# Optimization experiments

Measured on AMD Instinct MI355X. Metric: run time of the kernel, lower is better.

The kernel has to match this reference:

```python
import jax, jax.numpy as jnp
import numpy as np

V, D, CTX, NL = 32000, 1024, 2048, 2
B, T = 4, 2048
EPS = 1e-5


def _layer_norm(x, gamma, beta):
    mu = jnp.mean(x, axis=-1, keepdims=True)
    var = jnp.var(x, axis=-1, keepdims=True)  # biased, matches unbiased=False
    return gamma * (x - mu) / jnp.sqrt(var + EPS) + beta


def setup_inputs() -> dict:
    key = jax.random.key(0)
    ks = jax.random.split(key, 12)
    s = 0.02
    return {
        "x": jax.random.randint(ks[0], (B, T), 0, V),
        "emb": jax.random.normal(ks[1], (V, D), jnp.float32) * s,
        "pos": jax.random.normal(ks[2], (CTX, D), jnp.float32) * s,
        "wq": jax.random.normal(ks[3], (NL, D, D), jnp.float32) * s,
        "wk": jax.random.normal(ks[4], (NL, D, D), jnp.float32) * s,
        "wv": jax.random.normal(ks[5], (NL, D, D), jnp.float32) * s,
        "wo": jax.random.normal(ks[6], (NL, D, D), jnp.float32) * s,
        "wup": jax.random.normal(ks[7], (NL, D, 4 * D), jnp.float32) * s,
        "bup": jnp.zeros((NL, 4 * D), jnp.float32),
        "wdown": jax.random.normal(ks[8], (NL, 4 * D, D), jnp.float32) * s,
        "bdown": jnp.zeros((NL, D), jnp.float32),
        "ga": jnp.ones((NL, D), jnp.float32),
        "ba": jnp.zeros((NL, D), jnp.float32),
        "gm": jnp.ones((NL, D), jnp.float32),
        "bm": jnp.zeros((NL, D), jnp.float32),
    }


def reference(x, emb, pos, wq, wk, wv, wo, wup, bup, wdown, bdown, ga, ba, gm, bm):
    Bx, Tx = x.shape
    d_model = emb.shape[-1]
    inv_sqrt_d = 1.0 / jnp.sqrt(jnp.asarray(d_model, jnp.float32))
    h = emb[x] + pos[:Tx][None, :, :]           # [B,T,D]
    causal = jnp.tril(jnp.ones((Tx, Tx), bool))  # [T,T]
    neg_inf = jnp.asarray(-jnp.inf, h.dtype)
    n_layers = wq.shape[0]
    for l in range(n_layers):
        residual = h
        q = h @ wq[l]
        k = h @ wk[l]
        v = h @ wv[l]
        wei = jnp.einsum('btd,bsd->bts', q, k) * inv_sqrt_d  # [B,T,T]
        wei = jnp.where(causal[None], wei, neg_inf)
        attn = jax.nn.softmax(wei, axis=-1)
        out = jnp.einsum('bts,bsd->btd', attn, v)
        z = out @ wo[l]
        h = _layer_norm(residual + z, ga[l], ba[l])
        m = jax.nn.relu(h @ wup[l] + bup[l]) @ wdown[l] + bdown[l]
        h = _layer_norm(h + m, gm[l], bm[l])
    return h
```

## Files before the change

### kernel.cpp

```cpp
#include <hip/hip_runtime.h>
#include <stdint.h>

typedef unsigned short u16;
typedef short short8 __attribute__((ext_vector_type(8)));
typedef short short4v __attribute__((ext_vector_type(4)));
typedef float f32x4 __attribute__((ext_vector_type(4)));

#define DEV static __device__ __forceinline__

DEV u16 f2bf(float x) {
    union { float f; uint32_t u; } v; v.f = x;
    uint32_t r = v.u + 0x7FFFu + ((v.u >> 16) & 1u);
    return (u16)(r >> 16);
}
DEV float bf2f(u16 h) {
    union { uint32_t u; float f; } v; v.u = ((uint32_t)h) << 16;
    return v.f;
}

DEV void gload_lds16(const u16* g, u16* l) {
    __builtin_amdgcn_global_load_lds(
        (__attribute__((address_space(1))) void*)g,
        (__attribute__((address_space(3))) void*)l, 16, 0, 0);
}

enum { F_RELU = 1, F_ACCUM = 2, F_CSKIP = 4, F_CKLIM = 8 };

__global__ __launch_bounds__(256, 2)
void gemm_bt(const u16* __restrict__ A, const u16* __restrict__ B,
             float* __restrict__ Cf, u16* __restrict__ Cb,
             const float* __restrict__ bias,
             int M, int N, int K, int lda, int ldb, int ldc,
             long long sA, long long sB, long long sC,
             float scale, int flags)
{
    const int tm = blockIdx.x, tn = blockIdx.y, bz = blockIdx.z;
    if ((flags & F_CSKIP) && tn > tm) return;
    A += (long long)bz * sA;
    B += (long long)bz * sB;
    const long long coff = (long long)bz * sC;

    __shared__ u16 As[128 * 32];
    __shared__ u16 Bs[128 * 32];

    const int tid = threadIdx.x;
    const int lane = tid & 63, w = tid >> 6;
    const int wr = w >> 1, wc = w & 1;
    const int l15 = lane & 15, l4 = lane >> 4;

    f32x4 acc[4][4];
    const f32x4 z4 = {0.f, 0.f, 0.f, 0.f};
#pragma unroll
    for (int m = 0; m < 4; ++m)
#pragma unroll
        for (int n = 0; n < 4; ++n) acc[m][n] = z4;

    int kend = K;
    if (flags & F_CKLIM) { int ke = (tm + 1) * 128; if (ke < kend) kend = ke; }

    const u16* Abase = A + (long long)tm * 128 * lda;
    const u16* Bbase = B + (long long)tn * 128 * ldb;

    for (int k0 = 0; k0 < kend; k0 += 32) {
#pragma unroll
        for (int i = 0; i < 2; ++i) {
            const int e0 = (i * 4 + w) * 512;
            const int e  = e0 + lane * 8;
            const int row = e >> 5, col = e & 31;
            gload_lds16(Abase + (long long)row * lda + (k0 + col), (u16*)As + e0);
            gload_lds16(Bbase + (long long)row * ldb + (k0 + col), (u16*)Bs + e0);
        }
        __syncthreads();

        short8 af[4], bfr[4];
#pragma unroll
        for (int m = 0; m < 4; ++m)
            af[m] = *(const short8*)&As[(wr * 64 + m * 16 + l15) * 32 + l4 * 8];
#pragma unroll
        for (int n = 0; n < 4; ++n)
            bfr[n] = *(const short8*)&Bs[(wc * 64 + n * 16 + l15) * 32 + l4 * 8];
#pragma unroll
        for (int m = 0; m < 4; ++m)
#pragma unroll
            for (int n = 0; n < 4; ++n)
                acc[m][n] = __builtin_amdgcn_mfma_f32_16x16x32_bf16(af[m], bfr[n], acc[m][n], 0, 0, 0);
        __syncthreads();
    }

#pragma unroll
    for (int n = 0; n < 4; ++n) {
        const int c = tn * 128 + wc * 64 + n * 16 + l15;
        const float bv = bias ? bias[c] : 0.0f;
#pragma unroll
        for (int m = 0; m < 4; ++m) {
            const int r0 = tm * 128 + wr * 64 + m * 16 + l4 * 4;
#pragma unroll
            for (int j = 0; j < 4; ++j) {
                float v = acc[m][n][j] * scale + bv;
                if (flags & F_RELU) v = fmaxf(v, 0.0f);
                const long long off = coff + (long long)(r0 + j) * ldc + c;
                if (flags & F_ACCUM) v += Cf[off];
                if (Cf) Cf[off] = v;
                if (Cb) Cb[off] = f2bf(v);
            }
        }
    }
}

__global__ void transpose_f2b(const float* __restrict__ in, u16* __restrict__ out, int R, int C)
{
    __shared__ float tile[32][33];
    const int tx = threadIdx.x, ty = threadIdx.y;
    const int gx = blockIdx.x, gy = blockIdx.y;
#pragma unroll
    for (int i = 0; i < 4; ++i)
        tile[ty + i * 8][tx] = in[(long long)(gy * 32 + ty + i * 8) * C + gx * 32 + tx];
    __syncthreads();
#pragma unroll
    for (int i = 0; i < 4; ++i)
        out[(long long)(gx * 32 + ty + i * 8) * R + gy * 32 + tx] = f2bf(tile[tx][ty + i * 8]);
}

__global__ void transpose_b2b(const u16* __restrict__ in, u16* __restrict__ out,
                              int R, int C, long long sIn, long long sOut)
{
    __shared__ u16 tile[32][34];
    in  += (long long)blockIdx.z * sIn;
    out += (long long)blockIdx.z * sOut;
    const int tx = threadIdx.x, ty = threadIdx.y;
    const int gx = blockIdx.x, gy = blockIdx.y;
#pragma unroll
    for (int i = 0; i < 4; ++i)
        tile[ty + i * 8][tx] = in[(long long)(gy * 32 + ty + i * 8) * C + gx * 32 + tx];
    __syncthreads();
#pragma unroll
    for (int i = 0; i < 4; ++i)
        out[(long long)(gx * 32 + ty + i * 8) * R + gy * 32 + tx] = tile[tx][ty + i * 8];
}

__global__ __launch_bounds__(256)
void embed_kernel(const int* __restrict__ x, const float* __restrict__ emb,
                  const float* __restrict__ pos, float* __restrict__ h32, u16* __restrict__ hbf)
{
    const long long row = blockIdx.x;
    const int t = (int)(row & 2047);
    const int idx = x[row];
    const int tid = threadIdx.x;
    const float4 e = ((const float4*)(emb + (long long)idx * 1024))[tid];
    const float4 p = ((const float4*)(pos + (long long)t * 1024))[tid];
    float y0 = e.x + p.x, y1 = e.y + p.y, y2 = e.z + p.z, y3 = e.w + p.w;
    float4 o; o.x = y0; o.y = y1; o.z = y2; o.w = y3;
    ((float4*)(h32 + row * 1024))[tid] = o;
    short4v ob = { (short)f2bf(y0), (short)f2bf(y1), (short)f2bf(y2), (short)f2bf(y3) };
    *(short4v*)(hbf + row * 1024 + tid * 4) = ob;
}

__global__ __launch_bounds__(256)
void ln_kernel(const float* __restrict__ a, const float* __restrict__ b,
               const float* __restrict__ gamma, const float* __restrict__ beta,
               float* __restrict__ o32, u16* __restrict__ obf)
{
    const long long row = blockIdx.x;
    const int tid = threadIdx.x, lane = tid & 63, w = tid >> 6;
    const float4 xa = ((const float4*)(a + row * 1024))[tid];
    const float4 xb = ((const float4*)(b + row * 1024))[tid];
    float x0 = xa.x + xb.x, x1 = xa.y + xb.y, x2 = xa.z + xb.z, x3 = xa.w + xb.w;
    float s = x0 + x1 + x2 + x3;
    float q = x0 * x0 + x1 * x1 + x2 * x2 + x3 * x3;
#pragma unroll
    for (int o = 32; o; o >>= 1) { s += __shfl_xor(s, o, 64); q += __shfl_xor(q, o, 64); }
    __shared__ float red[8];
    if (lane == 0) { red[w] = s; red[4 + w] = q; }
    __syncthreads();
    s = red[0] + red[1] + red[2] + red[3];
    q = red[4] + red[5] + red[6] + red[7];
    const float mu = s * (1.0f / 1024.0f);
    const float var = q * (1.0f / 1024.0f) - mu * mu;
    const float rs = rsqrtf(var + 1e-5f);
    const float4 g  = ((const float4*)gamma)[tid];
    const float4 be = ((const float4*)beta)[tid];
    float y0 = (x0 - mu) * rs * g.x + be.x;
    float y1 = (x1 - mu) * rs * g.y + be.y;
    float y2 = (x2 - mu) * rs * g.z + be.z;
    float y3 = (x3 - mu) * rs * g.w + be.w;
    float4 o; o.x = y0; o.y = y1; o.z = y2; o.w = y3;
    ((float4*)(o32 + row * 1024))[tid] = o;
    short4v ob = { (short)f2bf(y0), (short)f2bf(y1), (short)f2bf(y2), (short)f2bf(y3) };
    *(short4v*)(obf + row * 1024 + tid * 4) = ob;
}

__global__ __launch_bounds__(256)
void softmax_causal(u16* __restrict__ SP)
{
    const long long row = blockIdx.x;
    const int t = (int)(row & 2047);
    u16* p = SP + row * 2048;
    const int tid = threadIdx.x, lane = tid & 63, w = tid >> 6;

    short8 v = *(const short8*)&p[tid * 8];
    float x[8];
#pragma unroll
    for (int j = 0; j < 8; ++j) {
        const int c = tid * 8 + j;
        x[j] = (c <= t) ? bf2f((u16)v[j]) : -1e30f;
    }
    float mx = x[0];
#pragma unroll
    for (int j = 1; j < 8; ++j) mx = fmaxf(mx, x[j]);
#pragma unroll
    for (int o = 32; o; o >>= 1) mx = fmaxf(mx, __shfl_xor(mx, o, 64));
    __shared__ float red[8];
    if (lane == 0) red[w] = mx;
    __syncthreads();
    mx = fmaxf(fmaxf(red[0], red[1]), fmaxf(red[2], red[3]));

    float s = 0.f;
#pragma unroll
    for (int j = 0; j < 8; ++j) {
        const float e = (tid * 8 + j <= t) ? exp2f((x[j] - mx) * 1.44269504f) : 0.f;
        x[j] = e; s += e;
    }
#pragma unroll
    for (int o = 32; o; o >>= 1) s += __shfl_xor(s, o, 64);
    if (lane == 0) red[4 + w] = s;
    __syncthreads();
    s = red[4] + red[5] + red[6] + red[7];
    const float inv = 1.0f / s;

    short8 ov;
#pragma unroll
    for (int j = 0; j < 8; ++j) ov[j] = (short)f2bf(x[j] * inv);
    *(short8*)&p[tid * 8] = ov;
}

extern "C" void kernel_launch(void* const* d_in, const int* in_sizes, int n_in,
                              void* d_out, int out_size, void* d_ws, size_t ws_size,
                              hipStream_t stream)
{
    (void)in_sizes; (void)n_in; (void)out_size; (void)ws_size;
    const int Dd = 1024, T_ = 2048, B_ = 4, NLl = 2, M = B_ * T_;
    const float inv_sqrt_d = 0.03125f;

    const int*   x     = (const int*)  d_in[0];
    const float* emb   = (const float*)d_in[1];
    const float* pos   = (const float*)d_in[2];
    const float* wq    = (const float*)d_in[3];
    const float* wk    = (const float*)d_in[4];
    const float* wv    = (const float*)d_in[5];
    const float* wo    = (const float*)d_in[6];
    const float* wup   = (const float*)d_in[7];
    const float* bup   = (const float*)d_in[8];
    const float* wdown = (const float*)d_in[9];
    const float* bdown = (const float*)d_in[10];
    const float* ga    = (const float*)d_in[11];
    const float* ba    = (const float*)d_in[12];
    const float* gm    = (const float*)d_in[13];
    const float* bm    = (const float*)d_in[14];

    char* ws = (char*)d_ws;
    size_t off = 0;
    auto alloc = [&](size_t bytes) -> void* {
        void* p = ws + off; off += (bytes + 255) & ~(size_t)255; return p;
    };
    float* h32  = (float*)alloc((size_t)M * Dd * 4);
    u16*   hbf  = (u16*)  alloc((size_t)M * Dd * 2);
    float* z32  = (float*)alloc((size_t)M * Dd * 4);
    u16*   qbf  = (u16*)  alloc((size_t)M * Dd * 2);
    u16*   kbf  = (u16*)  alloc((size_t)M * Dd * 2);
    u16*   vbf  = (u16*)  alloc((size_t)M * Dd * 2);
    u16*   vtbf = (u16*)  alloc((size_t)M * Dd * 2);
    u16*   SP   = (u16*)  alloc((size_t)B_ * T_ * T_ * 2);
    u16*   ubf  = (u16*)  alloc((size_t)M * 2048 * 2);
    u16*   wtb  = (u16*)  alloc((size_t)12 * 1024 * 1024 * 2);

    u16* wq_t    = wtb;
    u16* wk_t    = wtb + 1 * 1048576;
    u16* wv_t    = wtb + 2 * 1048576;
    u16* wo_t    = wtb + 3 * 1048576;
    u16* wup_t   = wtb + 4 * 1048576;
    u16* wdown_t = wtb + 8 * 1048576;

    dim3 blk(256);
    dim3 tblk(32, 8);

    embed_kernel<<<M, blk, 0, stream>>>(x, emb, pos, h32, hbf);

    for (int l = 0; l < NLl; ++l) {
        const float* wq_l    = wq    + (size_t)l * Dd * Dd;
        const float* wk_l    = wk    + (size_t)l * Dd * Dd;
        const float* wv_l    = wv    + (size_t)l * Dd * Dd;
        const float* wo_l    = wo    + (size_t)l * Dd * Dd;
        const float* wup_l   = wup   + (size_t)l * Dd * 4096;
        const float* wdown_l = wdown + (size_t)l * 4096 * Dd;

        transpose_f2b<<<dim3(32, 32),  tblk, 0, stream>>>(wq_l, wq_t, 1024, 1024);
        transpose_f2b<<<dim3(32, 32),  tblk, 0, stream>>>(wk_l, wk_t, 1024, 1024);
        transpose_f2b<<<dim3(32, 32),  tblk, 0, stream>>>(wv_l, wv_t, 1024, 1024);
        transpose_f2b<<<dim3(32, 32),  tblk, 0, stream>>>(wo_l, wo_t, 1024, 1024);
        transpose_f2b<<<dim3(128, 32), tblk, 0, stream>>>(wup_l, wup_t, 1024, 4096);
        transpose_f2b<<<dim3(32, 128), tblk, 0, stream>>>(wdown_l, wdown_t, 4096, 1024);

        gemm_bt<<<dim3(64, 8, 1), blk, 0, stream>>>(hbf, wq_t, nullptr, qbf, nullptr,
            M, 1024, 1024, 1024, 1024, 1024, 0, 0, 0, inv_sqrt_d, 0);
        gemm_bt<<<dim3(64, 8, 1), blk, 0, stream>>>(hbf, wk_t, nullptr, kbf, nullptr,
            M, 1024, 1024, 1024, 1024, 1024, 0, 0, 0, 1.0f, 0);
        gemm_bt<<<dim3(64, 8, 1), blk, 0, stream>>>(hbf, wv_t, nullptr, vbf, nullptr,
            M, 1024, 1024, 1024, 1024, 1024, 0, 0, 0, 1.0f, 0);

        transpose_b2b<<<dim3(32, 64, 4), tblk, 0, stream>>>(vbf, vtbf, 2048, 1024,
            (long long)T_ * Dd, (long long)T_ * Dd);

        gemm_bt<<<dim3(16, 16, 4), blk, 0, stream>>>(qbf, kbf, nullptr, SP, nullptr,
            2048, 2048, 1024, 1024, 1024, 2048,
            (long long)T_ * Dd, (long long)T_ * Dd, (long long)T_ * T_, 1.0f, F_CSKIP);

        softmax_causal<<<B_ * T_, blk, 0, stream>>>(SP);

        gemm_bt<<<dim3(16, 8, 4), blk, 0, stream>>>(SP, vtbf, nullptr, qbf, nullptr,
            2048, 1024, 2048, 2048, 2048, 1024,
            (long long)T_ * T_, (long long)Dd * T_, (long long)T_ * Dd, 1.0f, F_CKLIM);

        gemm_bt<<<dim3(64, 8, 1), blk, 0, stream>>>(qbf, wo_t, z32, nullptr, nullptr,
            M, 1024, 1024, 1024, 1024, 1024, 0, 0, 0, 1.0f, 0);

        ln_kernel<<<M, blk, 0, stream>>>(h32, z32, ga + (size_t)l * Dd, ba + (size_t)l * Dd, h32, hbf);

        for (int c = 0; c < 2; ++c) {
            gemm_bt<<<dim3(64, 16, 1), blk, 0, stream>>>(hbf, wup_t + (size_t)c * 2048 * 1024,
                nullptr, ubf, bup + (size_t)l * 4096 + c * 2048,
                M, 2048, 1024, 1024, 1024, 2048, 0, 0, 0, 1.0f, F_RELU);
            gemm_bt<<<dim3(64, 8, 1), blk, 0, stream>>>(ubf, wdown_t + (size_t)c * 2048,
                z32, nullptr, (c == 0) ? (bdown + (size_t)l * Dd) : nullptr,
                M, 1024, 2048, 2048, 4096, 1024, 0, 0, 0, 1.0f, (c == 0) ? 0 : F_ACCUM);
        }

        float* lnout = (l == NLl - 1) ? (float*)d_out : h32;
        ln_kernel<<<M, blk, 0, stream>>>(h32, z32, gm + (size_t)l * Dd, bm + (size_t)l * Dd, lnout, hbf);
    }
}
```

Measured before the change: 1.259 ms.

## Fuse QKV GEMM, batch weight transposes, split-K out/down projections, trim softmax

After: 1.207 ms. 4.1% less time.

```diff
diff --git a/kernel.cpp b/kernel.cpp
--- a/kernel.cpp
+++ b/kernel.cpp
@@ -24,7 +24,7 @@
         (__attribute__((address_space(3))) void*)l, 16, 0, 0);
 }
 
-enum { F_RELU = 1, F_ACCUM = 2, F_CSKIP = 4, F_CKLIM = 8 };
+enum { F_RELU = 1, F_CSKIP = 4, F_CKLIM = 8, F_BIAS0Z = 16, F_SPLITK = 32 };
 
 __global__ __launch_bounds__(256, 2)
 void gemm_bt(const u16* __restrict__ A, const u16* __restrict__ B,
@@ -90,7 +90,7 @@
 #pragma unroll
     for (int n = 0; n < 4; ++n) {
         const int c = tn * 128 + wc * 64 + n * 16 + l15;
-        const float bv = bias ? bias[c] : 0.0f;
+        const float bv = (bias && (!(flags & F_BIAS0Z) || bz == 0)) ? bias[c] : 0.0f;
 #pragma unroll
         for (int m = 0; m < 4; ++m) {
             const int r0 = tm * 128 + wr * 64 + m * 16 + l4 * 4;
@@ -99,7 +99,6 @@
                 float v = acc[m][n][j] * scale + bv;
                 if (flags & F_RELU) v = fmaxf(v, 0.0f);
                 const long long off = coff + (long long)(r0 + j) * ldc + c;
-                if (flags & F_ACCUM) v += Cf[off];
                 if (Cf) Cf[off] = v;
                 if (Cb) Cb[off] = f2bf(v);
             }
@@ -107,22 +106,49 @@
     }
 }
 
-__global__ void transpose_f2b(const float* __restrict__ in, u16* __restrict__ out, int R, int C)
-{
+__global__ void transpose_all(const float* __restrict__ wq, const float* __restrict__ wk,
+                              const float* __restrict__ wv, const float* __restrict__ wo,
+                              const float* __restrict__ wup, const float* __restrict__ wdown,
+                              u16* __restrict__ wqkv_t, u16* __restrict__ wo_t,
+                              u16* __restrict__ wup_t, u16* __restrict__ wdown_t,
+                              float qscale)
+{
+    const int gid = blockIdx.x, l = blockIdx.y;
+    const float* in;
+    u16* out;
+    int R, C, gx, gy;
+    float scale = 1.0f;
+
+    if (gid < 4096) {
+        const int seg = gid >> 10, widx = gid & 1023;
+        R = 1024; C = 1024; gx = widx & 31; gy = widx >> 5;
+        if (seg == 0)      { in = wq + (size_t)l * 1048576; out = wqkv_t + (size_t)l * 3145728;            scale = qscale; }
+        else if (seg == 1) { in = wk + (size_t)l * 1048576; out = wqkv_t + (size_t)l * 3145728 + 1048576; }
+        else if (seg == 2) { in = wv + (size_t)l * 1048576; out = wqkv_t + (size_t)l * 3145728 + 2097152; }
+        else               { in = wo + (size_t)l * 1048576; out = wo_t   + (size_t)l * 1048576; }
+    } else if (gid < 8192) {
+        const int widx = gid - 4096;
+        R = 1024; C = 4096; gx = widx & 127; gy = widx >> 7;
+        in = wup + (size_t)l * 4194304; out = wup_t + (size_t)l * 4194304;
+    } else {
+        const int widx = gid - 8192;
+        R = 4096; C = 1024; gx = widx & 31; gy = widx >> 5;
+        in = wdown + (size_t)l * 4194304; out = wdown_t + (size_t)l * 4194304;
+    }
+
     __shared__ float tile[32][33];
     const int tx = threadIdx.x, ty = threadIdx.y;
-    const int gx = blockIdx.x, gy = blockIdx.y;
 #pragma unroll
     for (int i = 0; i < 4; ++i)
         tile[ty + i * 8][tx] = in[(long long)(gy * 32 + ty + i * 8) * C + gx * 32 + tx];
     __syncthreads();
 #pragma unroll
     for (int i = 0; i < 4; ++i)
-        out[(long long)(gx * 32 + ty + i * 8) * R + gy * 32 + tx] = f2bf(tile[tx][ty + i * 8]);
+        out[(long long)(gx * 32 + ty + i * 8) * R + gy * 32 + tx] = f2bf(tile[tx][ty + i * 8] * scale);
 }
 
 __global__ void transpose_b2b(const u16* __restrict__ in, u16* __restrict__ out,
-                              int R, int C, long long sIn, long long sOut)
+                              int R, int C, int ldin, long long sIn, long long sOut)
 {
     __shared__ u16 tile[32][34];
     in  += (long long)blockIdx.z * sIn;
@@ -131,7 +157,7 @@
     const int gx = blockIdx.x, gy = blockIdx.y;
 #pragma unroll
     for (int i = 0; i < 4; ++i)
-        tile[ty + i * 8][tx] = in[(long long)(gy * 32 + ty + i * 8) * C + gx * 32 + tx];
+        tile[ty + i * 8][tx] = in[(long long)(gy * 32 + ty + i * 8) * ldin + gx * 32 + tx];
     __syncthreads();
 #pragma unroll
     for (int i = 0; i < 4; ++i)
@@ -157,6 +183,7 @@
 
 __global__ __launch_bounds__(256)
 void ln_kernel(const float* __restrict__ a, const float* __restrict__ b,
+               const float* __restrict__ c,
                const float* __restrict__ gamma, const float* __restrict__ beta,
                float* __restrict__ o32, u16* __restrict__ obf)
 {
@@ -165,6 +192,10 @@
     const float4 xa = ((const float4*)(a + row * 1024))[tid];
     const float4 xb = ((const float4*)(b + row * 1024))[tid];
     float x0 = xa.x + xb.x, x1 = xa.y + xb.y, x2 = xa.z + xb.z, x3 = xa.w + xb.w;
+    if (c) {
+        const float4 xc = ((const float4*)(c + row * 1024))[tid];
+        x0 += xc.x; x1 += xc.y; x2 += xc.z; x3 += xc.w;
+    }
     float s = x0 + x1 + x2 + x3;
     float q = x0 * x0 + x1 * x1 + x2 * x2 + x3 * x3;
 #pragma unroll
@@ -194,15 +225,18 @@
 {
     const long long row = blockIdx.x;
     const int t = (int)(row & 2047);
+    const int limit = ((t >> 7) + 1) << 7;
     u16* p = SP + row * 2048;
     const int tid = threadIdx.x, lane = tid & 63, w = tid >> 6;
-
-    short8 v = *(const short8*)&p[tid * 8];
+    const bool act = (tid * 8) < limit;
+
+    short8 v = {0, 0, 0, 0, 0, 0, 0, 0};
+    if (act) v = *(const short8*)&p[tid * 8];
     float x[8];
 #pragma unroll
     for (int j = 0; j < 8; ++j) {
-        const int c = tid * 8 + j;
-        x[j] = (c <= t) ? bf2f((u16)v[j]) : -1e30f;
+        const int cc = tid * 8 + j;
+        x[j] = (act && cc <= t) ? bf2f((u16)v[j]) : -1e30f;
     }
     float mx = x[0];
 #pragma unroll
@@ -217,7 +251,7 @@
     float s = 0.f;
 #pragma unroll
     for (int j = 0; j < 8; ++j) {
-        const float e = (tid * 8 + j <= t) ? exp2f((x[j] - mx) * 1.44269504f) : 0.f;
+        const float e = (act && tid * 8 + j <= t) ? exp2f((x[j] - mx) * 1.44269504f) : 0.f;
         x[j] = e; s += e;
     }
 #pragma unroll
@@ -227,10 +261,12 @@
     s = red[4] + red[5] + red[6] + red[7];
     const float inv = 1.0f / s;
 
-    short8 ov;
-#pragma unroll
-    for (int j = 0; j < 8; ++j) ov[j] = (short)f2bf(x[j] * inv);
-    *(short8*)&p[tid * 8] = ov;
+    if (act) {
+        short8 ov;
+#pragma unroll
+        for (int j = 0; j < 8; ++j) ov[j] = (short)f2bf(x[j] * inv);
+        *(short8*)&p[tid * 8] = ov;
+    }
 }
 
 extern "C" void kernel_launch(void* const* d_in, const int* in_sizes, int n_in,
@@ -262,79 +298,67 @@
     auto alloc = [&](size_t bytes) -> void* {
         void* p = ws + off; off += (bytes + 255) & ~(size_t)255; return p;
     };
-    float* h32  = (float*)alloc((size_t)M * Dd * 4);
-    u16*   hbf  = (u16*)  alloc((size_t)M * Dd * 2);
-    float* z32  = (float*)alloc((size_t)M * Dd * 4);
-    u16*   qbf  = (u16*)  alloc((size_t)M * Dd * 2);
-    u16*   kbf  = (u16*)  alloc((size_t)M * Dd * 2);
-    u16*   vbf  = (u16*)  alloc((size_t)M * Dd * 2);
-    u16*   vtbf = (u16*)  alloc((size_t)M * Dd * 2);
-    u16*   SP   = (u16*)  alloc((size_t)B_ * T_ * T_ * 2);
-    u16*   ubf  = (u16*)  alloc((size_t)M * 2048 * 2);
-    u16*   wtb  = (u16*)  alloc((size_t)12 * 1024 * 1024 * 2);
-
-    u16* wq_t    = wtb;
-    u16* wk_t    = wtb + 1 * 1048576;
-    u16* wv_t    = wtb + 2 * 1048576;
-    u16* wo_t    = wtb + 3 * 1048576;
-    u16* wup_t   = wtb + 4 * 1048576;
-    u16* wdown_t = wtb + 8 * 1048576;
+    float* h32   = (float*)alloc((size_t)M * Dd * 4);
+    u16*   hbf   = (u16*)  alloc((size_t)M * Dd * 2);
+    float* za    = (float*)alloc((size_t)M * Dd * 4);
+    float* zb    = (float*)alloc((size_t)M * Dd * 4);
+    u16*   qkv   = (u16*)  alloc((size_t)M * 3072 * 2);
+    u16*   abf   = (u16*)  alloc((size_t)M * Dd * 2);
+    u16*   vtbf  = (u16*)  alloc((size_t)M * Dd * 2);
+    u16*   SP    = (u16*)  alloc((size_t)B_ * T_ * T_ * 2);
+    u16*   ubf   = (u16*)  alloc((size_t)M * 4096 * 2);
+    u16*   wqkv_t  = (u16*)alloc((size_t)NLl * 3072 * 1024 * 2);
+    u16*   wo_t    = (u16*)alloc((size_t)NLl * 1024 * 1024 * 2);
+    u16*   wup_t   = (u16*)alloc((size_t)NLl * 4096 * 1024 * 2);
+    u16*   wdown_t = (u16*)alloc((size_t)NLl * 1024 * 4096 * 2);
+    const long long zstride = (long long)M * Dd;
 
     dim3 blk(256);
     dim3 tblk(32, 8);
 
+    transpose_all<<<dim3(12288, NLl), tblk, 0, stream>>>(wq, wk, wv, wo, wup, wdown,
+        wqkv_t, wo_t, wup_t, wdown_t, inv_sqrt_d);
+
     embed_kernel<<<M, blk, 0, stream>>>(x, emb, pos, h32, hbf);
 
     for (int l = 0; l < NLl; ++l) {
-        const float* wq_l    = wq    + (size_t)l * Dd * Dd;
-        const float* wk_l    = wk    + (size_t)l * Dd * Dd;
-        const float* wv_l    = wv    + (size_t)l * Dd * Dd;
-        const float* wo_l    = wo    + (size_t)l * Dd * Dd;
-        const float* wup_l   = wup   + (size_t)l * Dd * 4096;
-        const float* wdown_l = wdown + (size_t)l * 4096 * Dd;
-
-        transpose_f2b<<<dim3(32, 32),  tblk, 0, stream>>>(wq_l, wq_t, 1024, 1024);
-        transpose_f2b<<<dim3(32, 32),  tblk, 0, stream>>>(wk_l, wk_t, 1024, 1024);
-        transpose_f2b<<<dim3(32, 32),  tblk, 0, stream>>>(wv_l, wv_t, 1024, 1024);
-        transpose_f2b<<<dim3(32, 32),  tblk, 0, stream>>>(wo_l, wo_t, 1024, 1024);
-        transpose_f2b<<<dim3(128, 32), tblk, 0, stream>>>(wup_l, wup_t, 1024, 4096);
-        transpose_f2b<<<dim3(32, 128), tblk, 0, stream>>>(wdown_l, wdown_t, 4096, 1024);
-
-        gemm_bt<<<dim3(64, 8, 1), blk, 0, stream>>>(hbf, wq_t, nullptr, qbf, nullptr,
-            M, 1024, 1024, 1024, 1024, 1024, 0, 0, 0, inv_sqrt_d, 0);
-        gemm_bt<<<dim3(64, 8, 1), blk, 0, stream>>>(hbf, wk_t, nullptr, kbf, nullptr,
-            M, 1024, 1024, 1024, 1024, 1024, 0, 0, 0, 1.0f, 0);
-        gemm_bt<<<dim3(64, 8, 1), blk, 0, stream>>>(hbf, wv_t, nullptr, vbf, nullptr,
-            M, 1024, 1024, 1024, 1024, 1024, 0, 0, 0, 1.0f, 0);
-
-        transpose_b2b<<<dim3(32, 64, 4), tblk, 0, stream>>>(vbf, vtbf, 2048, 1024,
-            (long long)T_ * Dd, (long long)T_ * Dd);
-
-        gemm_bt<<<dim3(16, 16, 4), blk, 0, stream>>>(qbf, kbf, nullptr, SP, nullptr,
-            2048, 2048, 1024, 1024, 1024, 2048,
-            (long long)T_ * Dd, (long long)T_ * Dd, (long long)T_ * T_, 1.0f, F_CSKIP);
+        u16* wqkv_l  = wqkv_t  + (size_t)l * 3072 * 1024;
+        u16* wo_l    = wo_t    + (size_t)l * 1024 * 1024;
+        u16* wup_l   = wup_t   + (size_t)l * 4096 * 1024;
+        u16* wdown_l = wdown_t + (size_t)l * 1024 * 4096;
+
+        gemm_bt<<<dim3(64, 24, 1), blk, 0, stream>>>(hbf, wqkv_l, nullptr, qkv, nullptr,
+            M, 3072, 1024, 1024, 1024, 3072, 0, 0, 0, 1.0f, 0);
+
+        transpose_b2b<<<dim3(32, 64, 4), tblk, 0, stream>>>(qkv + 2048, vtbf, 2048, 1024,
+            3072, (long long)T_ * 3072, (long long)Dd * T_);
+
+        gemm_bt<<<dim3(16, 16, 4), blk, 0, stream>>>(qkv, qkv + 1024, nullptr, SP, nullptr,
+            2048, 2048, 1024, 3072, 3072, 2048,
+            (long long)T_ * 3072, (long long)T_ * 3072, (long long)T_ * T_, 1.0f, F_CSKIP);
 
         softmax_causal<<<B_ * T_, blk, 0, stream>>>(SP);
 
-        gemm_bt<<<dim3(16, 8, 4), blk, 0, stream>>>(SP, vtbf, nullptr, qbf, nullptr,
+        gemm_bt<<<dim3(16, 8, 4), blk, 0, stream>>>(SP, vtbf, nullptr, abf, nullptr,
             2048, 1024, 2048, 2048, 2048, 1024,
             (long long)T_ * T_, (long long)Dd * T_, (long long)T_ * Dd, 1.0f, F_CKLIM);
 
-        gemm_bt<<<dim3(64, 8, 1), blk, 0, stream>>>(qbf, wo_t, z32, nullptr, nullptr,
-            M, 1024, 1024, 1024, 1024, 1024, 0, 0, 0, 1.0f, 0);
-
-        ln_kernel<<<M, blk, 0, stream>>>(h32, z32, ga + (size_t)l * Dd, ba + (size_t)l * Dd, h32, hbf);
-
-        for (int c = 0; c < 2; ++c) {
-            gemm_bt<<<dim3(64, 16, 1), blk, 0, stream>>>(hbf, wup_t + (size_t)c * 2048 * 1024,
-                nullptr, ubf, bup + (size_t)l * 4096 + c * 2048,
-                M, 2048, 1024, 1024, 1024, 2048, 0, 0, 0, 1.0f, F_RELU);
-            gemm_bt<<<dim3(64, 8, 1), blk, 0, stream>>>(ubf, wdown_t + (size_t)c * 2048,
-                z32, nullptr, (c == 0) ? (bdown + (size_t)l * Dd) : nullptr,
-                M, 1024, 2048, 2048, 4096, 1024, 0, 0, 0, 1.0f, (c == 0) ? 0 : F_ACCUM);
-        }
+        gemm_bt<<<dim3(64, 8, 2), blk, 0, stream>>>(abf, wo_l, za, nullptr, nullptr,
+            M, 1024, 512, 1024, 1024, 1024, 512, 512, zstride, 1.0f, F_SPLITK);
+
+        ln_kernel<<<M, blk, 0, stream>>>(h32, za, zb,
+            ga + (size_t)l * Dd, ba + (size_t)l * Dd, h32, hbf);
+
+        gemm_bt<<<dim3(64, 32, 1), blk, 0, stream>>>(hbf, wup_l, nullptr, ubf,
+            bup + (size_t)l * 4096,
+            M, 4096, 1024, 1024, 1024, 4096, 0, 0, 0, 1.0f, F_RELU);
+
+        gemm_bt<<<dim3(64, 8, 2), blk, 0, stream>>>(ubf, wdown_l, za, nullptr,
+            bdown + (size_t)l * Dd,
+            M, 1024, 2048, 4096, 4096, 1024, 2048, 2048, zstride, 1.0f, F_SPLITK | F_BIAS0Z);
 
         float* lnout = (l == NLl - 1) ? (float*)d_out : h32;
-        ln_kernel<<<M, blk, 0, stream>>>(h32, z32, gm + (size_t)l * Dd, bm + (size_t)l * Dd, lnout, hbf);
-    }
-}
+        ln_kernel<<<M, blk, 0, stream>>>(h32, za, zb,
+            gm + (size_t)l * Dd, bm + (size_t)l * Dd, lnout, hbf);
+    }
+}
```
